# Kernel optimization log

Measured on AMD Instinct MI355X. Metric: run time of the kernel, lower is better.

The kernel has to match this reference:

```python
import jax, jax.numpy as jnp
import numpy as np

B, S, D = 1, 2048, 1024   # batch, seq_len, d_model
E, F, TOP_K = 8, 4096, 2  # num_experts, d_ff, top_k


def setup_inputs() -> dict:
    key = jax.random.key(0)
    k0, k1, k2, k3, k4 = jax.random.split(key, 5)
    s = 0.02
    x = jax.random.normal(k0, (B, S, D), jnp.float32)
    Wr = jax.random.normal(k1, (D, E), jnp.float32) * s          # router
    W1 = jax.random.normal(k2, (E, D, F), jnp.float32) * s       # gate proj per expert
    W3 = jax.random.normal(k3, (E, D, F), jnp.float32) * s       # up proj per expert
    W2 = jax.random.normal(k4, (E, F, D), jnp.float32) * s       # down proj per expert
    return {"x": x, "Wr": Wr, "W1": W1, "W2": W2, "W3": W3}


def reference(x, Wr, W1, W2, W3):
    b, s, d = x.shape
    e = Wr.shape[1]
    xt = x.reshape(b * s, d)                       # [T, D]
    logits = xt @ Wr                               # [T, E]
    top_v, top_i = jax.lax.top_k(logits, TOP_K)    # [T, K]
    probs = jax.nn.softmax(top_v, axis=-1)         # softmax over selected experts
    # combine[t, e] = prob of expert e for token t (0 if not selected)
    combine = jnp.sum(probs[..., None] * jax.nn.one_hot(top_i, e, dtype=xt.dtype), axis=1)  # [T, E]
    # SwiGLU FFN per expert (dense grouped-GEMM form of the gather/scatter loop)
    h = jnp.einsum('td,edf->etf', xt, W1)          # [E, T, F]
    g = jnp.einsum('td,edf->etf', xt, W3)          # [E, T, F]
    y = jnp.einsum('etf,efd->etd', jax.nn.silu(h) * g, W2)  # [E, T, D]
    out = jnp.einsum('etd,te->td', y, combine)     # weighted combine
    return out.reshape(b, s, d)
```

## Files before the change

kernel.cpp:

```cpp
#include <hip/hip_runtime.h>
#include <hip/hip_bf16.h>

#define T_TOK 2048
#define DDIM  1024
#define NEXP  8
#define FDIM  4096

typedef __attribute__((ext_vector_type(8))) short bf16x8;
typedef __attribute__((ext_vector_type(4))) float f32x4;

#define SBW(n) ((((n) >> 3) ^ (n)) & 7)

__device__ __forceinline__ unsigned short f2b(float f) {
  union { float f; unsigned u; } v; v.f = f;
  unsigned r = v.u + 0x7FFF + ((v.u >> 16) & 1);
  return (unsigned short)(r >> 16);
}
__device__ __forceinline__ float b2f(unsigned short s) {
  union { unsigned u; float f; } v; v.u = ((unsigned)s) << 16;
  return v.f;
}
__device__ __forceinline__ unsigned cvtpk(float lo, float hi) {
  unsigned r;
  asm("v_cvt_pk_bf16_f32 %0, %1, %2" : "=v"(r) : "v"(lo), "v"(hi));
  return r;
}

__device__ __forceinline__ void gl16(const unsigned short* g, unsigned short* l) {
  __builtin_amdgcn_global_load_lds(
      (const __attribute__((address_space(1))) unsigned int*)(const void*)g,
      (__attribute__((address_space(3))) unsigned int*)(void*)l, 16, 0, 0);
}

__global__ void router_kernel(const float* __restrict__ x, const float* __restrict__ Wr,
                              int* __restrict__ cnt, int* __restrict__ tok,
                              float* __restrict__ prb) {
  int t = (blockIdx.x * blockDim.x + threadIdx.x) >> 6;
  int lane = threadIdx.x & 63;
  if (t >= T_TOK) return;
  const float* xr = x + (size_t)t * DDIM;
  float acc[NEXP];
#pragma unroll
  for (int e = 0; e < NEXP; ++e) acc[e] = 0.f;
#pragma unroll
  for (int i = 0; i < 4; ++i) {
    int d0 = lane * 16 + i * 4;
    float4 xv = *reinterpret_cast<const float4*>(xr + d0);
#pragma unroll
    for (int j = 0; j < 4; ++j) {
      float xd = (&xv.x)[j];
      float4 w0 = *reinterpret_cast<const float4*>(Wr + (size_t)(d0 + j) * NEXP);
      float4 w1 = *reinterpret_cast<const float4*>(Wr + (size_t)(d0 + j) * NEXP + 4);
      acc[0] += xd * w0.x; acc[1] += xd * w0.y; acc[2] += xd * w0.z; acc[3] += xd * w0.w;
      acc[4] += xd * w1.x; acc[5] += xd * w1.y; acc[6] += xd * w1.z; acc[7] += xd * w1.w;
    }
  }
#pragma unroll
  for (int off = 32; off >= 1; off >>= 1)
#pragma unroll
    for (int e = 0; e < NEXP; ++e) acc[e] += __shfl_down(acc[e], off);
  if (lane == 0) {
    float v0 = -1e30f, v1 = -1e30f; int i0 = 0, i1 = 0;
#pragma unroll
    for (int e = 0; e < NEXP; ++e) {
      float v = acc[e];
      if (v > v0)      { v1 = v0; i1 = i0; v0 = v; i0 = e; }
      else if (v > v1) { v1 = v; i1 = e; }
    }
    float e1 = __expf(v1 - v0);
    float p0 = 1.f / (1.f + e1);
    float p1 = e1 * p0;
    int s0 = atomicAdd(&cnt[i0], 1);
    tok[i0 * T_TOK + s0] = t; prb[i0 * T_TOK + s0] = p0;
    int s1 = atomicAdd(&cnt[i1], 1);
    tok[i1 * T_TOK + s1] = t; prb[i1 * T_TOK + s1] = p1;
  }
}

__global__ void cvt_x_kernel(const float* __restrict__ in, unsigned short* __restrict__ o) {
  size_t i = ((size_t)blockIdx.x * 256 + threadIdx.x) * 8;
  float4 a = *reinterpret_cast<const float4*>(in + i);
  float4 b = *reinterpret_cast<const float4*>(in + i + 4);
  bf16x8 p;
  p[0] = (short)f2b(a.x); p[1] = (short)f2b(a.y); p[2] = (short)f2b(a.z); p[3] = (short)f2b(a.w);
  p[4] = (short)f2b(b.x); p[5] = (short)f2b(b.y); p[6] = (short)f2b(b.z); p[7] = (short)f2b(b.w);
  *reinterpret_cast<bf16x8*>(o + i) = p;
}

__global__ __launch_bounds__(256, 2)
void gemm1ab_kernel(const unsigned short* __restrict__ xb,
                    const float* __restrict__ W1, const float* __restrict__ W3,
                    const int* __restrict__ cnt, const int* __restrict__ tok,
                    unsigned short* __restrict__ act) {
  const int e = blockIdx.z;
  const int cn = cnt[e];
  const int r0 = blockIdx.y * 128;
  if (r0 >= cn) return;
  const int n0 = blockIdx.x * 64;
  int off = 0;
#pragma unroll
  for (int i = 0; i < NEXP; ++i) off += (i < e) ? cnt[i] : 0;

  __shared__ __align__(16) unsigned short sA[128 * 64];
  __shared__ __align__(16) unsigned short sB1[64 * 64];
  __shared__ __align__(16) unsigned short sB3[64 * 64];

  const int tid = threadIdx.x;
  const int lane = tid & 63;
  const int wid = tid >> 6;
  const int wm = wid >> 1, wn = wid & 1;

  const unsigned short* asrc[4];
#pragma unroll
  for (int i = 0; i < 4; ++i) {
    int row = (4 * wid + i) * 8 + (lane >> 3);
    int slot = r0 + row; if (slot >= cn) slot = cn - 1;
    int tk = tok[e * T_TOK + slot];
    int sl = (lane & 7) ^ (row & 7);
    asrc[i] = xb + (size_t)tk * DDIM + sl * 8;
  }

  const int kq = tid >> 4;
  const int nc = (tid & 15) * 4;
  const float* b1p = W1 + ((size_t)e * DDIM + 4 * kq) * FDIM + n0 + nc;
  const float* b3p = W3 + ((size_t)e * DDIM + 4 * kq) * FDIM + n0 + nc;

  float4 r1[4], r3[4];
#pragma unroll
  for (int r = 0; r < 4; ++r) {
    r1[r] = *reinterpret_cast<const float4*>(b1p + (size_t)r * FDIM);
    r3[r] = *reinterpret_cast<const float4*>(b3p + (size_t)r * FDIM);
  }

  f32x4 ah[4][2], ag[4][2];
#pragma unroll
  for (int m = 0; m < 4; ++m)
#pragma unroll
    for (int n = 0; n < 2; ++n) { ah[m][n] = (f32x4){0,0,0,0}; ag[m][n] = (f32x4){0,0,0,0}; }

  for (int k0 = 0; k0 < DDIM; k0 += 64) {
#pragma unroll
    for (int j = 0; j < 4; ++j) {
      int n = nc + j;
      int offB = n * 128 + (((kq >> 1) ^ SBW(n)) * 16) + (kq & 1) * 8;
      uint2 wv;
      wv.x = cvtpk((&r1[0].x)[j], (&r1[1].x)[j]);
      wv.y = cvtpk((&r1[2].x)[j], (&r1[3].x)[j]);
      *reinterpret_cast<uint2*>((char*)sB1 + offB) = wv;
      wv.x = cvtpk((&r3[0].x)[j], (&r3[1].x)[j]);
      wv.y = cvtpk((&r3[2].x)[j], (&r3[3].x)[j]);
      *reinterpret_cast<uint2*>((char*)sB3 + offB) = wv;
    }
#pragma unroll
    for (int i = 0; i < 4; ++i) gl16(asrc[i] + k0, &sA[(4 * wid + i) * 512]);
    __syncthreads();
    if (k0 + 64 < DDIM) {
#pragma unroll
      for (int r = 0; r < 4; ++r) {
        r1[r] = *reinterpret_cast<const float4*>(b1p + (size_t)(k0 + 64 + r) * FDIM);
        r3[r] = *reinterpret_cast<const float4*>(b3p + (size_t)(k0 + 64 + r) * FDIM);
      }
    }
#pragma unroll
    for (int kk = 0; kk < 2; ++kk) {
      int kc8 = kk * 4 + (lane >> 4);
      bf16x8 a[4], b1[2], b3[2];
#pragma unroll
      for (int m = 0; m < 4; ++m) {
        int row = wm * 64 + m * 16 + (lane & 15);
        a[m] = *reinterpret_cast<const bf16x8*>(&sA[row * 64 + ((kc8 ^ (row & 7)) * 8)]);
      }
#pragma unroll
      for (int n = 0; n < 2; ++n) {
        int rowb = wn * 32 + n * 16 + (lane & 15);
        int offb = rowb * 64 + ((kc8 ^ SBW(rowb)) * 8);
        b1[n] = *reinterpret_cast<const bf16x8*>(&sB1[offb]);
        b3[n] = *reinterpret_cast<const bf16x8*>(&sB3[offb]);
      }
#pragma unroll
      for (int m = 0; m < 4; ++m)
#pragma unroll
        for (int n = 0; n < 2; ++n) {
          ah[m][n] = __builtin_amdgcn_mfma_f32_16x16x32_bf16(a[m], b1[n], ah[m][n], 0, 0, 0);
          ag[m][n] = __builtin_amdgcn_mfma_f32_16x16x32_bf16(a[m], b3[n], ag[m][n], 0, 0, 0);
        }
    }
    __syncthreads();
  }
#pragma unroll
  for (int m = 0; m < 4; ++m)
#pragma unroll
    for (int j = 0; j < 4; ++j) {
      int rloc = wm * 64 + m * 16 + (lane >> 4) * 4 + j;
      int s = r0 + rloc;
      if (s < cn) {
        unsigned short* orow = act + (size_t)(off + s) * FDIM + n0 + wn * 32 + (lane & 15);
#pragma unroll
        for (int n = 0; n < 2; ++n) {
          float hv = ah[m][n][j];
          float gv = ag[m][n][j];
          float sg = hv / (1.f + __expf(-hv));
          orow[n * 16] = f2b(sg * gv);
        }
      }
    }
}

__global__ __launch_bounds__(256, 2)
void gemm2d_kernel(const unsigned short* __restrict__ act, const float* __restrict__ W2,
                   const int* __restrict__ cnt, const int* __restrict__ tok,
                   const float* __restrict__ prb, float* __restrict__ out) {
  const int e = blockIdx.z >> 2;
  const int sp = blockIdx.z & 3;
  const int cn = cnt[e];
  const int r0 = blockIdx.y * 128;
  if (r0 >= cn) return;
  const int n0 = blockIdx.x * 128;
  const int kbase = sp * (FDIM / 4);
  int off = 0;
#pragma unroll
  for (int i = 0; i < NEXP; ++i) off += (i < e) ? cnt[i] : 0;

  __shared__ __align__(16) unsigned short sA[128 * 64];
  __shared__ __align__(16) unsigned short sB[128 * 64];

  const int tid = threadIdx.x;
  const int lane = tid & 63;
  const int wid = tid >> 6;
  const int wm = wid >> 1, wn = wid & 1;

  const unsigned short* asrc[4];
#pragma unroll
  for (int i = 0; i < 4; ++i) {
    int row = (4 * wid + i) * 8 + (lane >> 3);
    int sl = (lane & 7) ^ (row & 7);
    asrc[i] = act + (size_t)(off + r0 + row) * FDIM + kbase + sl * 8;
  }

  const int kq = tid >> 4;
  const int nc = (tid & 15) * 8;
  const float* b2p = W2 + ((size_t)e * FDIM + kbase + 4 * kq) * DDIM + n0 + nc;

  float4 ra[4], rb[4];
#pragma unroll
  for (int r = 0; r < 4; ++r) {
    ra[r] = *reinterpret_cast<const float4*>(b2p + (size_t)r * DDIM);
    rb[r] = *reinterpret_cast<const float4*>(b2p + (size_t)r * DDIM + 4);
  }

  f32x4 acc[4][4];
#pragma unroll
  for (int m = 0; m < 4; ++m)
#pragma unroll
    for (int n = 0; n < 4; ++n) acc[m][n] = (f32x4){0,0,0,0};

  for (int k0 = 0; k0 < FDIM / 4; k0 += 64) {
#pragma unroll
    for (int j = 0; j < 8; ++j) {
      int n = nc + j;
      int offB = n * 128 + (((kq >> 1) ^ SBW(n)) * 16) + (kq & 1) * 8;
      uint2 wv;
      if (j < 4) {
        wv.x = cvtpk((&ra[0].x)[j], (&ra[1].x)[j]);
        wv.y = cvtpk((&ra[2].x)[j], (&ra[3].x)[j]);
      } else {
        wv.x = cvtpk((&rb[0].x)[j - 4], (&rb[1].x)[j - 4]);
        wv.y = cvtpk((&rb[2].x)[j - 4], (&rb[3].x)[j - 4]);
      }
      *reinterpret_cast<uint2*>((char*)sB + offB) = wv;
    }
#pragma unroll
    for (int i = 0; i < 4; ++i) gl16(asrc[i] + k0, &sA[(4 * wid + i) * 512]);
    __syncthreads();
    if (k0 + 64 < FDIM / 4) {
#pragma unroll
      for (int r = 0; r < 4; ++r) {
        ra[r] = *reinterpret_cast<const float4*>(b2p + (size_t)(k0 + 64 + r) * DDIM);
        rb[r] = *reinterpret_cast<const float4*>(b2p + (size_t)(k0 + 64 + r) * DDIM + 4);
      }
    }
#pragma unroll
    for (int kk = 0; kk < 2; ++kk) {
      int kc8 = kk * 4 + (lane >> 4);
      bf16x8 a[4], b[4];
#pragma unroll
      for (int m = 0; m < 4; ++m) {
        int row = wm * 64 + m * 16 + (lane & 15);
        a[m] = *reinterpret_cast<const bf16x8*>(&sA[row * 64 + ((kc8 ^ (row & 7)) * 8)]);
      }
#pragma unroll
      for (int n = 0; n < 4; ++n) {
        int rowb = wn * 64 + n * 16 + (lane & 15);
        b[n] = *reinterpret_cast<const bf16x8*>(&sB[rowb * 64 + ((kc8 ^ SBW(rowb)) * 8)]);
      }
#pragma unroll
      for (int m = 0; m < 4; ++m)
#pragma unroll
        for (int n = 0; n < 4; ++n)
          acc[m][n] = __builtin_amdgcn_mfma_f32_16x16x32_bf16(a[m], b[n], acc[m][n], 0, 0, 0);
    }
    __syncthreads();
  }
#pragma unroll
  for (int m = 0; m < 4; ++m)
#pragma unroll
    for (int j = 0; j < 4; ++j) {
      int rloc = wm * 64 + m * 16 + (lane >> 4) * 4 + j;
      int s = r0 + rloc;
      if (s < cn) {
        int tkn = tok[e * T_TOK + s];
        float p = prb[e * T_TOK + s];
        float* orow = out + (size_t)tkn * DDIM + n0 + wn * 64 + (lane & 15);
#pragma unroll
        for (int n = 0; n < 4; ++n) atomicAdd(&orow[n * 16], p * acc[m][n][j]);
      }
    }
}

extern "C" void kernel_launch(void* const* d_in, const int* in_sizes, int n_in,
                              void* d_out, int out_size, void* d_ws, size_t ws_size,
                              hipStream_t stream) {
  const float* x  = (const float*)d_in[0];
  const float* Wr = (const float*)d_in[1];
  const float* W1 = (const float*)d_in[2];
  const float* W2 = (const float*)d_in[3];
  const float* W3 = (const float*)d_in[4];
  float* out = (float*)d_out;

  char* ws = (char*)d_ws;
  int*   cnt = (int*)ws;
  int*   tok = (int*)(ws + 1024);
  float* prb = (float*)(ws + 1024 + 65536);
  unsigned short* xb  = (unsigned short*)(ws + 256 * 1024);
  unsigned short* act = xb + (size_t)T_TOK * DDIM;

  hipMemsetAsync(cnt, 0, NEXP * sizeof(int), stream);
  hipMemsetAsync(d_out, 0, (size_t)out_size * sizeof(float), stream);

  router_kernel<<<T_TOK / 4, 256, 0, stream>>>(x, Wr, cnt, tok, prb);
  cvt_x_kernel<<<(T_TOK * DDIM) / (256 * 8), 256, 0, stream>>>(x, xb);
  gemm1ab_kernel<<<dim3(FDIM / 64, 16, NEXP), 256, 0, stream>>>(xb, W1, W3, cnt, tok, act);
  gemm2d_kernel<<<dim3(DDIM / 128, 16, NEXP * 4), 256, 0, stream>>>(act, W2, cnt, tok, prb, out);
}
```

Baseline: 307.7 us.

## Double-buffer LDS tiles in both expert GEMMs with one-stage-ahead B register prefetch

Both expert GEMM kernels now keep two LDS buffers for the A and B tiles. Each iteration stages the next tile (async A load into LDS, converted B weights written from registers) while the current tile feeds the MFMAs, and global B loads run two tiles ahead. This is meant to remove the serialization between the LDS fill and compute within each k-step. The B staging layout also changes: each thread now loads 8 k-rows and writes full 16-byte bf16x8 chunks instead of 8-byte halves, and in gemm1 the W1 and W3 loads are split between thread halves. The cost is twice the LDS per block, which may limit occupancy with launch_bounds(256,2), plus more registers.

```diff
diff --git a/kernel.cpp b/kernel.cpp
--- a/kernel.cpp
+++ b/kernel.cpp
@@ -25,11 +25,18 @@
   asm("v_cvt_pk_bf16_f32 %0, %1, %2" : "=v"(r) : "v"(lo), "v"(hi));
   return r;
 }
-
 __device__ __forceinline__ void gl16(const unsigned short* g, unsigned short* l) {
   __builtin_amdgcn_global_load_lds(
       (const __attribute__((address_space(1))) unsigned int*)(const void*)g,
       (__attribute__((address_space(3))) unsigned int*)(void*)l, 16, 0, 0);
+}
+__device__ __forceinline__ bf16x8 pack8(const float4* br, int c) {
+  union { bf16x8 v; unsigned u[4]; } p;
+  p.u[0] = cvtpk((&br[0].x)[c], (&br[1].x)[c]);
+  p.u[1] = cvtpk((&br[2].x)[c], (&br[3].x)[c]);
+  p.u[2] = cvtpk((&br[4].x)[c], (&br[5].x)[c]);
+  p.u[3] = cvtpk((&br[6].x)[c], (&br[7].x)[c]);
+  return p.v;
 }
 
 __global__ void router_kernel(const float* __restrict__ x, const float* __restrict__ Wr,
@@ -101,9 +108,9 @@
 #pragma unroll
   for (int i = 0; i < NEXP; ++i) off += (i < e) ? cnt[i] : 0;
 
-  __shared__ __align__(16) unsigned short sA[128 * 64];
-  __shared__ __align__(16) unsigned short sB1[64 * 64];
-  __shared__ __align__(16) unsigned short sB3[64 * 64];
+  __shared__ __align__(16) unsigned short sA[2][128 * 64];
+  __shared__ __align__(16) unsigned short sB1[2][64 * 64];
+  __shared__ __align__(16) unsigned short sB3[2][64 * 64];
 
   const int tid = threadIdx.x;
   const int lane = tid & 63;
@@ -120,17 +127,25 @@
     asrc[i] = xb + (size_t)tk * DDIM + sl * 8;
   }
 
-  const int kq = tid >> 4;
-  const int nc = (tid & 15) * 4;
-  const float* b1p = W1 + ((size_t)e * DDIM + 4 * kq) * FDIM + n0 + nc;
-  const float* b3p = W3 + ((size_t)e * DDIM + 4 * kq) * FDIM + n0 + nc;
-
-  float4 r1[4], r3[4];
-#pragma unroll
-  for (int r = 0; r < 4; ++r) {
-    r1[r] = *reinterpret_cast<const float4*>(b1p + (size_t)r * FDIM);
-    r3[r] = *reinterpret_cast<const float4*>(b3p + (size_t)r * FDIM);
-  }
+  const int lt = tid & 127;
+  const int ko = lt >> 4;
+  const int nc = (lt & 15) * 4;
+  const float* bp = ((tid < 128) ? W1 : W3) + ((size_t)e * DDIM + 8 * ko) * FDIM + n0 + nc;
+  unsigned short* wb = (tid < 128) ? &sB1[0][0] : &sB3[0][0];
+  int woff[4];
+#pragma unroll
+  for (int c = 0; c < 4; ++c) woff[c] = (nc + c) * 64 + ((ko ^ SBW(nc + c)) * 8);
+
+  float4 br[8];
+#define LOADB1(K0)                                                              \
+  _Pragma("unroll") for (int r = 0; r < 8; ++r)                                 \
+      br[r] = *reinterpret_cast<const float4*>(bp + (size_t)((K0) + r) * FDIM);
+#define WRITEB1(BUF)                                                            \
+  _Pragma("unroll") for (int c = 0; c < 4; ++c)                                 \
+      *reinterpret_cast<bf16x8*>(wb + (BUF) * 4096 + woff[c]) = pack8(br, c);
+#define STAGEA1(K0, BUF)                                                        \
+  _Pragma("unroll") for (int i = 0; i < 4; ++i)                                 \
+      gl16(asrc[i] + (K0), &sA[BUF][(4 * wid + i) * 512]);
 
   f32x4 ah[4][2], ag[4][2];
 #pragma unroll
@@ -138,28 +153,19 @@
 #pragma unroll
     for (int n = 0; n < 2; ++n) { ah[m][n] = (f32x4){0,0,0,0}; ag[m][n] = (f32x4){0,0,0,0}; }
 
-  for (int k0 = 0; k0 < DDIM; k0 += 64) {
-#pragma unroll
-    for (int j = 0; j < 4; ++j) {
-      int n = nc + j;
-      int offB = n * 128 + (((kq >> 1) ^ SBW(n)) * 16) + (kq & 1) * 8;
-      uint2 wv;
-      wv.x = cvtpk((&r1[0].x)[j], (&r1[1].x)[j]);
-      wv.y = cvtpk((&r1[2].x)[j], (&r1[3].x)[j]);
-      *reinterpret_cast<uint2*>((char*)sB1 + offB) = wv;
-      wv.x = cvtpk((&r3[0].x)[j], (&r3[1].x)[j]);
-      wv.y = cvtpk((&r3[2].x)[j], (&r3[3].x)[j]);
-      *reinterpret_cast<uint2*>((char*)sB3 + offB) = wv;
-    }
-#pragma unroll
-    for (int i = 0; i < 4; ++i) gl16(asrc[i] + k0, &sA[(4 * wid + i) * 512]);
-    __syncthreads();
+  LOADB1(0);
+  STAGEA1(0, 0);
+  WRITEB1(0);
+  LOADB1(64);
+  __syncthreads();
+
+  int cur = 0;
+  for (int k0 = 0; k0 < DDIM; k0 += 64, cur ^= 1) {
+    const int nxt = cur ^ 1;
     if (k0 + 64 < DDIM) {
-#pragma unroll
-      for (int r = 0; r < 4; ++r) {
-        r1[r] = *reinterpret_cast<const float4*>(b1p + (size_t)(k0 + 64 + r) * FDIM);
-        r3[r] = *reinterpret_cast<const float4*>(b3p + (size_t)(k0 + 64 + r) * FDIM);
-      }
+      STAGEA1(k0 + 64, nxt);
+      WRITEB1(nxt);
+      if (k0 + 128 < DDIM) LOADB1(k0 + 128);
     }
 #pragma unroll
     for (int kk = 0; kk < 2; ++kk) {
@@ -168,14 +174,14 @@
 #pragma unroll
       for (int m = 0; m < 4; ++m) {
         int row = wm * 64 + m * 16 + (lane & 15);
-        a[m] = *reinterpret_cast<const bf16x8*>(&sA[row * 64 + ((kc8 ^ (row & 7)) * 8)]);
+        a[m] = *reinterpret_cast<const bf16x8*>(&sA[cur][row * 64 + ((kc8 ^ (row & 7)) * 8)]);
       }
 #pragma unroll
       for (int n = 0; n < 2; ++n) {
         int rowb = wn * 32 + n * 16 + (lane & 15);
         int offb = rowb * 64 + ((kc8 ^ SBW(rowb)) * 8);
-        b1[n] = *reinterpret_cast<const bf16x8*>(&sB1[offb]);
-        b3[n] = *reinterpret_cast<const bf16x8*>(&sB3[offb]);
+        b1[n] = *reinterpret_cast<const bf16x8*>(&sB1[cur][offb]);
+        b3[n] = *reinterpret_cast<const bf16x8*>(&sB3[cur][offb]);
       }
 #pragma unroll
       for (int m = 0; m < 4; ++m)
@@ -221,8 +227,8 @@
 #pragma unroll
   for (int i = 0; i < NEXP; ++i) off += (i < e) ? cnt[i] : 0;
 
-  __shared__ __align__(16) unsigned short sA[128 * 64];
-  __shared__ __align__(16) unsigned short sB[128 * 64];
+  __shared__ __align__(16) unsigned short sA[2][128 * 64];
+  __shared__ __align__(16) unsigned short sB[2][128 * 64];
 
   const int tid = threadIdx.x;
   const int lane = tid & 63;
@@ -237,16 +243,23 @@
     asrc[i] = act + (size_t)(off + r0 + row) * FDIM + kbase + sl * 8;
   }
 
-  const int kq = tid >> 4;
-  const int nc = (tid & 15) * 8;
-  const float* b2p = W2 + ((size_t)e * FDIM + kbase + 4 * kq) * DDIM + n0 + nc;
-
-  float4 ra[4], rb[4];
-#pragma unroll
-  for (int r = 0; r < 4; ++r) {
-    ra[r] = *reinterpret_cast<const float4*>(b2p + (size_t)r * DDIM);
-    rb[r] = *reinterpret_cast<const float4*>(b2p + (size_t)r * DDIM + 4);
-  }
+  const int ko = tid >> 5;
+  const int nc = (tid & 31) * 4;
+  const float* bp = W2 + ((size_t)e * FDIM + kbase + 8 * ko) * DDIM + n0 + nc;
+  int woff[4];
+#pragma unroll
+  for (int c = 0; c < 4; ++c) woff[c] = (nc + c) * 64 + ((ko ^ SBW(nc + c)) * 8);
+
+  float4 br[8];
+#define LOADB2(K0)                                                              \
+  _Pragma("unroll") for (int r = 0; r < 8; ++r)                                 \
+      br[r] = *reinterpret_cast<const float4*>(bp + (size_t)((K0) + r) * DDIM);
+#define WRITEB2(BUF)                                                            \
+  _Pragma("unroll") for (int c = 0; c < 4; ++c)                                 \
+      *reinterpret_cast<bf16x8*>(&sB[BUF][woff[c]]) = pack8(br, c);
+#define STAGEA2(K0, BUF)                                                        \
+  _Pragma("unroll") for (int i = 0; i < 4; ++i)                                 \
+      gl16(asrc[i] + (K0), &sA[BUF][(4 * wid + i) * 512]);
 
   f32x4 acc[4][4];
 #pragma unroll
@@ -254,30 +267,19 @@
 #pragma unroll
     for (int n = 0; n < 4; ++n) acc[m][n] = (f32x4){0,0,0,0};
 
-  for (int k0 = 0; k0 < FDIM / 4; k0 += 64) {
-#pragma unroll
-    for (int j = 0; j < 8; ++j) {
-      int n = nc + j;
-      int offB = n * 128 + (((kq >> 1) ^ SBW(n)) * 16) + (kq & 1) * 8;
-      uint2 wv;
-      if (j < 4) {
-        wv.x = cvtpk((&ra[0].x)[j], (&ra[1].x)[j]);
-        wv.y = cvtpk((&ra[2].x)[j], (&ra[3].x)[j]);
-      } else {
-        wv.x = cvtpk((&rb[0].x)[j - 4], (&rb[1].x)[j - 4]);
-        wv.y = cvtpk((&rb[2].x)[j - 4], (&rb[3].x)[j - 4]);
-      }
-      *reinterpret_cast<uint2*>((char*)sB + offB) = wv;
-    }
-#pragma unroll
-    for (int i = 0; i < 4; ++i) gl16(asrc[i] + k0, &sA[(4 * wid + i) * 512]);
-    __syncthreads();
+  LOADB2(0);
+  STAGEA2(0, 0);
+  WRITEB2(0);
+  LOADB2(64);
+  __syncthreads();
+
+  int cur = 0;
+  for (int k0 = 0; k0 < FDIM / 4; k0 += 64, cur ^= 1) {
+    const int nxt = cur ^ 1;
     if (k0 + 64 < FDIM / 4) {
-#pragma unroll
-      for (int r = 0; r < 4; ++r) {
-        ra[r] = *reinterpret_cast<const float4*>(b2p + (size_t)(k0 + 64 + r) * DDIM);
-        rb[r] = *reinterpret_cast<const float4*>(b2p + (size_t)(k0 + 64 + r) * DDIM + 4);
-      }
+      STAGEA2(k0 + 64, nxt);
+      WRITEB2(nxt);
+      if (k0 + 128 < FDIM / 4) LOADB2(k0 + 128);
     }
 #pragma unroll
     for (int kk = 0; kk < 2; ++kk) {
@@ -286,12 +288,12 @@
 #pragma unroll
       for (int m = 0; m < 4; ++m) {
         int row = wm * 64 + m * 16 + (lane & 15);
-        a[m] = *reinterpret_cast<const bf16x8*>(&sA[row * 64 + ((kc8 ^ (row & 7)) * 8)]);
+        a[m] = *reinterpret_cast<const bf16x8*>(&sA[cur][row * 64 + ((kc8 ^ (row & 7)) * 8)]);
       }
 #pragma unroll
       for (int n = 0; n < 4; ++n) {
         int rowb = wn * 64 + n * 16 + (lane & 15);
-        b[n] = *reinterpret_cast<const bf16x8*>(&sB[rowb * 64 + ((kc8 ^ SBW(rowb)) * 8)]);
+        b[n] = *reinterpret_cast<const bf16x8*>(&sB[cur][rowb * 64 + ((kc8 ^ SBW(rowb)) * 8)]);
       }
 #pragma unroll
       for (int m = 0; m < 4; ++m)
```

Measured after the change: 322.4 us. +4.8%, slower.
